# Kernel tuning notes

Hardware: AMD Instinct MI355X
Metric: run time of the kernel (lower is better)

## Reference

```python
import jax, jax.numpy as jnp
import numpy as np

ALPHA, BETA, GAMMA = 1.0, 0.01, 0.1
COS_EPS = 1e-8  # torch F.cosine_similarity eps


def setup_inputs() -> dict:
    key = jax.random.key(0)
    k1, k2, k3, k4 = jax.random.split(key, 4)
    B, C = 4096, 1000
    N, D = 8192, 256
    return {
        "pred": jax.random.normal(k1, (B, C), dtype=jnp.float32),
        "target": jax.random.randint(k2, (B,), 0, C, dtype=jnp.int64),
        "adj_matrix": jax.random.uniform(k3, (N, N), dtype=jnp.float32),
        "node_embeddings": jax.random.normal(k4, (N, D), dtype=jnp.float32),
    }


def reference(pred, target, adj_matrix, node_embeddings):
    # L_task: mean cross-entropy over logits
    logp = jax.nn.log_softmax(pred, axis=-1)                      # [B, C]
    l_task = -jnp.mean(jnp.take_along_axis(logp, target[:, None], axis=1))

    # L_sparse: mean |adj|
    l_sparse = jnp.mean(jnp.abs(adj_matrix))

    # L_semantic: cosine similarity via normalize + matmul (avoids NxNxD intermediate)
    norms = jnp.linalg.norm(node_embeddings, axis=1)              # [N]
    dots = node_embeddings @ node_embeddings.T                    # [N, N]
    sim = dots / jnp.maximum(norms[:, None] * norms[None, :], COS_EPS)
    l_semantic = jnp.mean(adj_matrix * (1.0 - sim))

    return ALPHA * l_task + BETA * l_sparse + GAMMA * l_semantic
```

## Files before the change

kernel.cpp:

```cpp
#include <hip/hip_runtime.h>
#include <hip/hip_bf16.h>
#include <stdint.h>
#include <stddef.h>

#define N_NODES 8192
#define DIM     256
#define BATCH   4096
#define CLASSES 1000
#define ALPHA_C 1.0f
#define BETA_C  0.01f
#define GAMMA_C 0.1f

typedef __bf16 bf16_t;
typedef __bf16 bf16x8 __attribute__((ext_vector_type(8)));
typedef float  f32x4  __attribute__((ext_vector_type(4)));
typedef float  f32x16 __attribute__((ext_vector_type(16)));

__device__ __forceinline__ void async16(const void* g, void* l) {
  __builtin_amdgcn_global_load_lds(
      (const __attribute__((address_space(1))) uint32_t*)g,
      (__attribute__((address_space(3))) uint32_t*)l, 16, 0, 0);
}

__global__ __launch_bounds__(256) void prep_kernel(
    const float* __restrict__ emb, bf16_t* __restrict__ U) {
  const int row = blockIdx.x;
  const int t = threadIdx.x;
  const float v = emb[(size_t)row * DIM + t];
  float sq = v * v;
  for (int off = 32; off; off >>= 1) sq += __shfl_down(sq, off);
  __shared__ float red[4];
  if ((t & 63) == 0) red[t >> 6] = sq;
  __syncthreads();
  const float total = red[0] + red[1] + red[2] + red[3];
  U[(size_t)row * DIM + t] = (bf16_t)(v * rsqrtf(total));
}

__global__ __launch_bounds__(256) void ce_kernel(
    const float* __restrict__ pred, const int* __restrict__ target,
    float* __restrict__ out) {
  const int row = blockIdx.x;
  const int t = threadIdx.x;
  const float* p = pred + (size_t)row * CLASSES;

  float v[4];
  for (int k = 0; k < 4; ++k) {
    const int c = t + k * 256;
    v[k] = (c < CLASSES) ? p[c] : -INFINITY;
  }

  float m = fmaxf(fmaxf(v[0], v[1]), fmaxf(v[2], v[3]));
  for (int off = 32; off; off >>= 1) m = fmaxf(m, __shfl_down(m, off));

  __shared__ float red[8];
  const int wave = t >> 6, lane = t & 63;
  if (lane == 0) red[wave] = m;
  __syncthreads();
  if (t == 0) red[4] = fmaxf(fmaxf(red[0], red[1]), fmaxf(red[2], red[3]));
  __syncthreads();
  const float mx = red[4];

  float s = 0.f;
  for (int k = 0; k < 4; ++k) s += __expf(v[k] - mx);
  for (int off = 32; off; off >>= 1) s += __shfl_down(s, off);
  if (lane == 0) red[wave] = s;
  __syncthreads();
  if (t == 0) {
    float ssum = red[0] + red[1] + red[2] + red[3];
    float lse = mx + __logf(ssum);
    float loss = lse - p[target[row]];
    atomicAdd(out, loss * (ALPHA_C / (float)BATCH));
  }
}

#define BT 128

__global__ __launch_bounds__(256, 3) void gram_kernel(
    const float* __restrict__ adj, const bf16_t* __restrict__ U,
    float* __restrict__ out) {
  __shared__ __align__(16) float lds_f[128 * 68];
  __shared__ float red[4];
  bf16_t* As = (bf16_t*)lds_f;
  bf16_t* Bs = ((bf16_t*)lds_f) + 128 * 64;

  const int bi = blockIdx.y, bj = blockIdx.x;
  const int i0 = bi * BT, j0 = bj * BT;
  const int t = threadIdx.x;
  const int w = t >> 6, lane = t & 63;
  const int wr = (w >> 1) * 64, wc = (w & 1) * 64;
  const int m = lane & 31, h = lane >> 5;

  const int srow = lane >> 3;
  const int schunk = (lane & 7) ^ srow;

  f32x16 acc[2][2] = {};

  for (int kc = 0; kc < 4; ++kc) {
    const int ko = kc * 64;
#pragma unroll
    for (int ii = 0; ii < 4; ++ii) {
      const int rbase = w * 32 + ii * 8;
      async16(U + (size_t)(i0 + rbase + srow) * DIM + ko + schunk * 8,
              &As[rbase * 64]);
      async16(U + (size_t)(j0 + rbase + srow) * DIM + ko + schunk * 8,
              &Bs[rbase * 64]);
    }
    __syncthreads();
#pragma unroll
    for (int kk = 0; kk < 64; kk += 16) {
      const int p = (((kk >> 3) + h) ^ (m & 7)) * 8;
      bf16x8 a0 = *(const bf16x8*)&As[(wr + m) * 64 + p];
      bf16x8 a1 = *(const bf16x8*)&As[(wr + 32 + m) * 64 + p];
      bf16x8 b0 = *(const bf16x8*)&Bs[(wc + m) * 64 + p];
      bf16x8 b1 = *(const bf16x8*)&Bs[(wc + 32 + m) * 64 + p];
      acc[0][0] =
          __builtin_amdgcn_mfma_f32_32x32x16_bf16(a0, b0, acc[0][0], 0, 0, 0);
      acc[0][1] =
          __builtin_amdgcn_mfma_f32_32x32x16_bf16(a0, b1, acc[0][1], 0, 0, 0);
      acc[1][0] =
          __builtin_amdgcn_mfma_f32_32x32x16_bf16(a1, b0, acc[1][0], 0, 0, 0);
      acc[1][1] =
          __builtin_amdgcn_mfma_f32_32x32x16_bf16(a1, b1, acc[1][1], 0, 0, 0);
    }
    __syncthreads();
  }

  float local = 0.f;
  const int g4 = t & 15;
  const int i_rel = ((g4 & 8) ? 64 : 0) + (g4 & 7) * 4;

#pragma unroll
  for (int ms = 0; ms < 2; ++ms) {
#pragma unroll
    for (int ns = 0; ns < 2; ++ns) {
      const int c = wc + ns * 32 + m;
#pragma unroll
      for (int rg = 0; rg < 4; ++rg) {
        const int rh = (w >> 1) * 32 + rg * 8 + h * 4;
        f32x4 vv = {acc[ms][ns][rg * 4 + 0], acc[ms][ns][rg * 4 + 1],
                    acc[ms][ns][rg * 4 + 2], acc[ms][ns][rg * 4 + 3]};
        *(f32x4*)&lds_f[c * 68 + rh] = vv;
      }
    }
    __syncthreads();
    const int i_off = ms * 32 + i_rel;
#pragma unroll
    for (int k = 0; k < 8; ++k) {
      const int c = (t >> 4) + k * 16;
      const f32x4 s = *(const f32x4*)&lds_f[c * 68 + g4 * 4];
      const float4 a4 =
          *(const float4*)&adj[(size_t)(j0 + c) * N_NODES + i0 + i_off];
      local +=
          BETA_C * (fabsf(a4.x) + fabsf(a4.y) + fabsf(a4.z) + fabsf(a4.w));
      local += GAMMA_C * (a4.x * (1.f - s.x) + a4.y * (1.f - s.y) +
                          a4.z * (1.f - s.z) + a4.w * (1.f - s.w));
    }
    __syncthreads();
  }

  for (int off = 32; off; off >>= 1) local += __shfl_down(local, off);
  if (lane == 0) red[w] = local;
  __syncthreads();
  if (t == 0) {
    const float inv = 1.f / ((float)N_NODES * (float)N_NODES);
    atomicAdd(out, (red[0] + red[1] + red[2] + red[3]) * inv);
  }
}

extern "C" void kernel_launch(void* const* d_in, const int* in_sizes, int n_in,
                              void* d_out, int out_size, void* d_ws,
                              size_t ws_size, hipStream_t stream) {
  const float* pred   = (const float*)d_in[0];
  const int*   target = (const int*)d_in[1];
  const float* adj    = (const float*)d_in[2];
  const float* emb    = (const float*)d_in[3];
  float* out = (float*)d_out;

  bf16_t* U = (bf16_t*)d_ws;

  hipMemsetAsync(d_out, 0, sizeof(float), stream);
  prep_kernel<<<N_NODES, 256, 0, stream>>>(emb, U);
  ce_kernel<<<BATCH, 256, 0, stream>>>(pred, target, out);
  gram_kernel<<<dim3(N_NODES / BT, N_NODES / BT), 256, 0, stream>>>(adj, U,
                                                                    out);
}
```

Baseline: 469.4 us.

## Reassociate semantic loss as trace of U^T A U instead of full Gram matrix

Rewrites sum(adj * U U^T) as the trace of U^T (adj U). Each block multiplies a 64-row slice of adj, converted to bf16, by a K-chunk of transposed U, then dots the result with U rows. This drops the N×N×D Gram GEMM and its epilogue in favour of an N×N×D product that streams adj once through MFMA, and adds a transpose kernel for U. It also rounds adj to bf16 inside the MFMA, which adds approximation error to the semantic term.

```diff
diff --git a/kernel.cpp b/kernel.cpp
--- a/kernel.cpp
+++ b/kernel.cpp
@@ -13,6 +13,7 @@
 
 typedef __bf16 bf16_t;
 typedef __bf16 bf16x8 __attribute__((ext_vector_type(8)));
+typedef __bf16 bf16x4 __attribute__((ext_vector_type(4)));
 typedef float  f32x4  __attribute__((ext_vector_type(4)));
 typedef float  f32x16 __attribute__((ext_vector_type(16)));
 
@@ -36,6 +37,29 @@
   U[(size_t)row * DIM + t] = (bf16_t)(v * rsqrtf(total));
 }
 
+__global__ __launch_bounds__(256) void transpose_kernel(
+    const bf16_t* __restrict__ U, bf16_t* __restrict__ Ut) {
+  __shared__ bf16_t tile[64][72];
+  const int i0 = blockIdx.x * 64, d0 = blockIdx.y * 64;
+  const int t = threadIdx.x;
+  const int r = t >> 3, c8 = (t & 7) * 8;
+#pragma unroll
+  for (int it = 0; it < 2; ++it) {
+    const int row = r + it * 32;
+    *(bf16x8*)&tile[row][c8] =
+        *(const bf16x8*)&U[(size_t)(i0 + row) * DIM + d0 + c8];
+  }
+  __syncthreads();
+#pragma unroll
+  for (int it = 0; it < 2; ++it) {
+    const int d = r + it * 32;
+    bf16x8 v;
+#pragma unroll
+    for (int j = 0; j < 8; ++j) v[j] = tile[c8 + j][d];
+    *(bf16x8*)&Ut[(size_t)(d0 + d) * N_NODES + i0 + c8] = v;
+  }
+}
+
 __global__ __launch_bounds__(256) void ce_kernel(
     const float* __restrict__ pred, const int* __restrict__ target,
     float* __restrict__ out) {
@@ -73,93 +97,102 @@
   }
 }
 
-#define BT 128
-
-__global__ __launch_bounds__(256, 3) void gram_kernel(
+#define BN 64
+#define BK 64
+#define KC 8
+#define KW (N_NODES / KC)
+#define NCHUNK (KW / BK)
+
+__global__ __launch_bounds__(256, 3) void semantic_kernel(
     const float* __restrict__ adj, const bf16_t* __restrict__ U,
-    float* __restrict__ out) {
-  __shared__ __align__(16) float lds_f[128 * 68];
+    const bf16_t* __restrict__ Ut, float* __restrict__ out) {
+  __shared__ __align__(16) bf16_t lds_ut[DIM * BK];
+  __shared__ __align__(16) float  lds_a[BN * BK];
   __shared__ float red[4];
-  bf16_t* As = (bf16_t*)lds_f;
-  bf16_t* Bs = ((bf16_t*)lds_f) + 128 * 64;
-
-  const int bi = blockIdx.y, bj = blockIdx.x;
-  const int i0 = bi * BT, j0 = bj * BT;
+
   const int t = threadIdx.x;
   const int w = t >> 6, lane = t & 63;
-  const int wr = (w >> 1) * 64, wc = (w & 1) * 64;
+  const int wm = w >> 1, wn = w & 1;
   const int m = lane & 31, h = lane >> 5;
-
-  const int srow = lane >> 3;
-  const int schunk = (lane & 7) ^ srow;
-
-  f32x16 acc[2][2] = {};
-
-  for (int kc = 0; kc < 4; ++kc) {
-    const int ko = kc * 64;
+  const int i0 = blockIdx.x * BN;
+  const int k0 = blockIdx.y * KW;
+
+  f32x16 acc[4] = {};
+  float s_abs = 0.f, s_sum = 0.f;
+
+  const int ut_rl = lane >> 3;
+  const int ut_c = (lane & 7) ^ ut_rl;
+  const int a_rl = lane >> 4;
+
+  for (int ck = 0; ck < NCHUNK; ++ck) {
+    const int ko = k0 + ck * BK;
+#pragma unroll
+    for (int ii = 0; ii < 8; ++ii) {
+      const int rbase = ii * 32 + w * 8;
+      async16(Ut + (size_t)(rbase + ut_rl) * N_NODES + ko + ut_c * 8,
+              &lds_ut[rbase * BK]);
+    }
 #pragma unroll
     for (int ii = 0; ii < 4; ++ii) {
-      const int rbase = w * 32 + ii * 8;
-      async16(U + (size_t)(i0 + rbase + srow) * DIM + ko + schunk * 8,
-              &As[rbase * 64]);
-      async16(U + (size_t)(j0 + rbase + srow) * DIM + ko + schunk * 8,
-              &Bs[rbase * 64]);
+      const int rbase = w * 16 + ii * 4;
+      const int r = rbase + a_rl;
+      const int c = (lane & 15) ^ (r & 15);
+      async16(adj + (size_t)(i0 + r) * N_NODES + ko + c * 4,
+              &lds_a[rbase * BK]);
     }
     __syncthreads();
 #pragma unroll
-    for (int kk = 0; kk < 64; kk += 16) {
-      const int p = (((kk >> 3) + h) ^ (m & 7)) * 8;
-      bf16x8 a0 = *(const bf16x8*)&As[(wr + m) * 64 + p];
-      bf16x8 a1 = *(const bf16x8*)&As[(wr + 32 + m) * 64 + p];
-      bf16x8 b0 = *(const bf16x8*)&Bs[(wc + m) * 64 + p];
-      bf16x8 b1 = *(const bf16x8*)&Bs[(wc + 32 + m) * 64 + p];
-      acc[0][0] =
-          __builtin_amdgcn_mfma_f32_32x32x16_bf16(a0, b0, acc[0][0], 0, 0, 0);
-      acc[0][1] =
-          __builtin_amdgcn_mfma_f32_32x32x16_bf16(a0, b1, acc[0][1], 0, 0, 0);
-      acc[1][0] =
-          __builtin_amdgcn_mfma_f32_32x32x16_bf16(a1, b0, acc[1][0], 0, 0, 0);
-      acc[1][1] =
-          __builtin_amdgcn_mfma_f32_32x32x16_bf16(a1, b1, acc[1][1], 0, 0, 0);
+    for (int kk = 0; kk < 4; ++kk) {
+      bf16x8 af[4];
+#pragma unroll
+      for (int mr = 0; mr < 4; ++mr) {
+        const int rd = wm * 128 + mr * 32 + m;
+        af[mr] = *(const bf16x8*)
+            &lds_ut[rd * BK + (((kk * 2 + h) ^ (rd & 7)) * 8)];
+      }
+      const int ri = wn * 32 + m;
+      const int c0 = kk * 4 + h * 2;
+      const f32x4 b0 =
+          *(const f32x4*)&lds_a[ri * BK + ((c0 ^ (ri & 15)) * 4)];
+      const f32x4 b1 =
+          *(const f32x4*)&lds_a[ri * BK + (((c0 + 1) ^ (ri & 15)) * 4)];
+      if (wm == 0) {
+        s_abs += fabsf(b0[0]) + fabsf(b0[1]) + fabsf(b0[2]) + fabsf(b0[3]) +
+                 fabsf(b1[0]) + fabsf(b1[1]) + fabsf(b1[2]) + fabsf(b1[3]);
+        s_sum += b0[0] + b0[1] + b0[2] + b0[3] + b1[0] + b1[1] + b1[2] + b1[3];
+      }
+      bf16x8 bb;
+      bb[0] = (bf16_t)b0[0]; bb[1] = (bf16_t)b0[1];
+      bb[2] = (bf16_t)b0[2]; bb[3] = (bf16_t)b0[3];
+      bb[4] = (bf16_t)b1[0]; bb[5] = (bf16_t)b1[1];
+      bb[6] = (bf16_t)b1[2]; bb[7] = (bf16_t)b1[3];
+#pragma unroll
+      for (int mr = 0; mr < 4; ++mr)
+        acc[mr] = __builtin_amdgcn_mfma_f32_32x32x16_bf16(af[mr], bb, acc[mr],
+                                                          0, 0, 0);
     }
     __syncthreads();
   }
 
-  float local = 0.f;
-  const int g4 = t & 15;
-  const int i_rel = ((g4 & 8) ? 64 : 0) + (g4 & 7) * 4;
-
-#pragma unroll
-  for (int ms = 0; ms < 2; ++ms) {
-#pragma unroll
-    for (int ns = 0; ns < 2; ++ns) {
-      const int c = wc + ns * 32 + m;
-#pragma unroll
-      for (int rg = 0; rg < 4; ++rg) {
-        const int rh = (w >> 1) * 32 + rg * 8 + h * 4;
-        f32x4 vv = {acc[ms][ns][rg * 4 + 0], acc[ms][ns][rg * 4 + 1],
-                    acc[ms][ns][rg * 4 + 2], acc[ms][ns][rg * 4 + 3]};
-        *(f32x4*)&lds_f[c * 68 + rh] = vv;
-      }
-    }
-    __syncthreads();
-    const int i_off = ms * 32 + i_rel;
-#pragma unroll
-    for (int k = 0; k < 8; ++k) {
-      const int c = (t >> 4) + k * 16;
-      const f32x4 s = *(const f32x4*)&lds_f[c * 68 + g4 * 4];
-      const float4 a4 =
-          *(const float4*)&adj[(size_t)(j0 + c) * N_NODES + i0 + i_off];
-      local +=
-          BETA_C * (fabsf(a4.x) + fabsf(a4.y) + fabsf(a4.z) + fabsf(a4.w));
-      local += GAMMA_C * (a4.x * (1.f - s.x) + a4.y * (1.f - s.y) +
-                          a4.z * (1.f - s.z) + a4.w * (1.f - s.w));
-    }
-    __syncthreads();
-  }
-
-  for (int off = 32; off; off >>= 1) local += __shfl_down(local, off);
-  if (lane == 0) red[w] = local;
+  float tr = 0.f;
+  const bf16_t* Urow = U + (size_t)(i0 + wn * 32 + m) * DIM;
+#pragma unroll
+  for (int mr = 0; mr < 4; ++mr) {
+#pragma unroll
+    for (int rq = 0; rq < 4; ++rq) {
+      const int d = wm * 128 + mr * 32 + rq * 8 + h * 4;
+      const bf16x4 uu = *(const bf16x4*)&Urow[d];
+      tr += acc[mr][rq * 4 + 0] * (float)uu[0] +
+            acc[mr][rq * 4 + 1] * (float)uu[1] +
+            acc[mr][rq * 4 + 2] * (float)uu[2] +
+            acc[mr][rq * 4 + 3] * (float)uu[3];
+    }
+  }
+
+  float contrib = -GAMMA_C * tr;
+  if (wm == 0) contrib += BETA_C * s_abs + GAMMA_C * s_sum;
+  for (int off = 32; off; off >>= 1) contrib += __shfl_down(contrib, off);
+  if (lane == 0) red[w] = contrib;
   __syncthreads();
   if (t == 0) {
     const float inv = 1.f / ((float)N_NODES * (float)N_NODES);
@@ -176,11 +209,12 @@
   const float* emb    = (const float*)d_in[3];
   float* out = (float*)d_out;
 
-  bf16_t* U = (bf16_t*)d_ws;
+  bf16_t* U  = (bf16_t*)d_ws;
+  bf16_t* Ut = U + (size_t)N_NODES * DIM;
 
   hipMemsetAsync(d_out, 0, sizeof(float), stream);
   prep_kernel<<<N_NODES, 256, 0, stream>>>(emb, U);
+  transpose_kernel<<<dim3(N_NODES / 64, DIM / 64), 256, 0, stream>>>(U, Ut);
   ce_kernel<<<BATCH, 256, 0, stream>>>(pred, target, out);
-  gram_kernel<<<dim3(N_NODES / BT, N_NODES / BT), 256, 0, stream>>>(adj, U,
-                                                                    out);
-}
+  semantic_kernel<<<dim3(N_NODES / BN, KC), 256, 0, stream>>>(adj, U, Ut, out);
+}
```

After: 490.9 us. 4.6% more time.
